# Optimization experiments

Hardware: AMD Instinct MI355X
Metric: run time of the kernel (lower is better)

The kernel has to match this reference:

```python
import jax, jax.numpy as jnp
import numpy as np

ALPHA_LO = float(np.exp(-1.0 / 5.0))   # 0.81873...
ALPHA_HI = float(np.exp(-1.0 / 25.0))  # 0.96079...
T_CROP = 0


def setup_inputs() -> dict:
    key = jax.random.key(0)
    k1, k2, k3, k4 = jax.random.split(key, 4)
    B, T, I, H = 64, 2000, 512, 512
    x = jax.random.normal(k1, (B, T, I), dtype=jnp.float32)
    # W ~ U(-sqrt(1/I), sqrt(1/I)) per nn.init.uniform_
    lim = float(np.sqrt(1.0 / I))
    W = jax.random.uniform(k2, (H, I), dtype=jnp.float32, minval=-lim, maxval=lim)
    # alpha ~ U(alpha_lim[0], alpha_lim[1])
    alpha = jax.random.uniform(k3, (H,), dtype=jnp.float32, minval=ALPHA_LO, maxval=ALPHA_HI)
    # initial membrane potential ~ U(0,1) (torch.rand in _readout_cell)
    u0 = jax.random.uniform(k4, (B, H), dtype=jnp.float32)
    return {"x": x, "W": W, "alpha": alpha, "u0": u0}


def reference(x, W, alpha, u0):
    # x: [B, T, I], W: [H, I] -> Wx: [B, T, H]
    alpha_c = jnp.clip(alpha, ALPHA_LO, ALPHA_HI)  # [H]
    beta = 1.0 - alpha_c                           # [H]
    Wx = jnp.einsum("bti,hi->bth", x, W)          # [B, T, H]
    Wx_t = jnp.swapaxes(Wx, 0, 1)                  # [T, B, H] for scan

    out0 = jnp.zeros_like(u0)

    def step(carry, inp):
        ut, out, t = carry
        wx_t = inp  # [B, H]
        ut = alpha_c * ut + beta * wx_t
        out = out + jnp.where(t >= T_CROP, jax.nn.softmax(ut, axis=1), 0.0)
        return (ut, out, t + 1), None

    (_, out, _), _ = jax.lax.scan(step, (u0, out0, jnp.int32(0)), Wx_t)
    return out  # [B, H]
```

## Files before the change

kernel.cpp:

```cpp
#include <hip/hip_runtime.h>
#include <hip/hip_bf16.h>
#include <stdint.h>

#define ALPHA_LO 0.8187307530779818f
#define ALPHA_HI 0.9607894391523232f

#define BATCH 64
#define TT    2000
#define II    512
#define HH    512
#define MM    (BATCH*TT)
#define LCH   50
#define CCH   (TT/LCH)

typedef __bf16 bf16;
typedef bf16  bf16x8 __attribute__((ext_vector_type(8)));
typedef float f32x4  __attribute__((ext_vector_type(4)));

#define GLDS(src, dst) __builtin_amdgcn_global_load_lds( \
    (const __attribute__((address_space(1))) unsigned int*)(src), \
    (__attribute__((address_space(3))) unsigned int*)(dst), 16, 0, 0)

__global__ void k_convW(const float* __restrict__ W, bf16* __restrict__ Wbt) {
    const int t  = blockIdx.x * 256 + threadIdx.x;
    const int h  = t >> 6;
    const int kb = t & 63;
    const float* src = W + (size_t)h * II + kb * 8;
    float4 v0 = *(const float4*)(src);
    float4 v1 = *(const float4*)(src + 4);
    bf16x8 o;
    o[0]=(bf16)v0.x; o[1]=(bf16)v0.y; o[2]=(bf16)v0.z; o[3]=(bf16)v0.w;
    o[4]=(bf16)v1.x; o[5]=(bf16)v1.y; o[6]=(bf16)v1.z; o[7]=(bf16)v1.w;
    const int ks = kb >> 2, kq = kb & 3, jj = h >> 4, fr = h & 15;
    bf16* dst = Wbt + (size_t)ks * 16384 + jj * 512 + kq * 128 + fr * 8;
    *(bf16x8*)dst = o;
}

__global__ __launch_bounds__(512, 2) void k_gemm(const float* __restrict__ X,
                                                 const bf16* __restrict__ Wbt,
                                                 bf16* __restrict__ Y) {
    __shared__ bf16 Al[2][4096];
    __shared__ bf16 Bl[4][16384];
    const int tid  = threadIdx.x;
    const int m0   = blockIdx.x * 128;
    const int lane = tid & 63;
    const int wv   = tid >> 6;
    const int wr   = (wv >> 2) * 64;
    const int wcj  = (wv & 3) * 8;
    const int wblk = (wv >> 2) * 4;
    const int fr   = lane & 15;
    const int kq   = lane >> 4;

    f32x4 acc[4][8] = {};

    const int arow = ((tid >> 6) << 4) + (tid & 15);
    const int akq  = (tid >> 4) & 3;
    const float* xa = X + (size_t)(m0 + arow) * II + akq * 8;
    const int aoff = tid * 8;

    const bf16* wsrc = Wbt + wv * 512 + lane * 8;

    float4 av[3][2];

    #pragma unroll
    for (int q = 0; q < 4; ++q) GLDS(wsrc + q * 4096,         &Bl[0][(q * 8 + wv) * 512]);
    av[0][0] = *(const float4*)(xa);
    av[0][1] = *(const float4*)(xa + 4);
    #pragma unroll
    for (int q = 0; q < 4; ++q) GLDS(wsrc + 16384 + q * 4096, &Bl[1][(q * 8 + wv) * 512]);
    av[1][0] = *(const float4*)(xa + 32);
    av[1][1] = *(const float4*)(xa + 36);

    #pragma unroll
    for (int ks = 0; ks < 16; ++ks) {
        const int bcur = ks & 3;
        const int acur = ks & 1;
        const int rcur = ks % 3;
        if (ks + 2 < 16) {
            #pragma unroll
            for (int q = 0; q < 4; ++q)
                GLDS(wsrc + (size_t)(ks + 2) * 16384 + q * 4096,
                     &Bl[(ks + 2) & 3][(q * 8 + wv) * 512]);
            av[(ks + 2) % 3][0] = *(const float4*)(xa + (size_t)(ks + 2) * 32);
            av[(ks + 2) % 3][1] = *(const float4*)(xa + (size_t)(ks + 2) * 32 + 4);
        }
        float4 a0 = av[rcur][0], a1 = av[rcur][1];
        bf16x8 c;
        c[0]=(bf16)a0.x; c[1]=(bf16)a0.y; c[2]=(bf16)a0.z; c[3]=(bf16)a0.w;
        c[4]=(bf16)a1.x; c[5]=(bf16)a1.y; c[6]=(bf16)a1.z; c[7]=(bf16)a1.w;
        *(bf16x8*)(&Al[acur][aoff]) = c;
        asm volatile("s_waitcnt lgkmcnt(0)" ::: "memory");
        __builtin_amdgcn_s_barrier();
        bf16x8 af[4], bb[8];
        #pragma unroll
        for (int i = 0; i < 4; ++i)
            af[i] = *(const bf16x8*)(&Al[acur][(wblk + i) * 512 + lane * 8]);
        #pragma unroll
        for (int j = 0; j < 8; ++j)
            bb[j] = *(const bf16x8*)(&Bl[bcur][(wcj + j) * 512 + lane * 8]);
        __builtin_amdgcn_s_setprio(1);
        #pragma unroll
        for (int i = 0; i < 4; ++i)
            #pragma unroll
            for (int j = 0; j < 8; ++j)
                acc[i][j] = __builtin_amdgcn_mfma_f32_16x16x32_bf16(af[i], bb[j], acc[i][j], 0, 0, 0);
        __builtin_amdgcn_s_setprio(0);
        asm volatile("" ::: "memory");
    }

    #pragma unroll
    for (int i = 0; i < 4; ++i)
        #pragma unroll
        for (int j = 0; j < 8; ++j) {
            const int row = m0 + wr + i * 16 + kq * 4;
            const int col = (wcj + j) * 16 + fr;
            #pragma unroll
            for (int r = 0; r < 4; ++r)
                Y[(size_t)(row + r) * HH + col] = (bf16)acc[i][j][r];
        }
}

__global__ void k_chunk(const bf16* __restrict__ Y, const float* __restrict__ alpha,
                        float* __restrict__ P) {
    const int c = blockIdx.x, b = blockIdx.y;
    const int lane = threadIdx.x;
    const int h0 = lane * 8;
    float a[8], p[8];
    #pragma unroll
    for (int k = 0; k < 8; ++k) {
        a[k] = fminf(fmaxf(alpha[h0 + k], ALPHA_LO), ALPHA_HI);
        p[k] = 0.f;
    }
    const bf16* base = Y + ((size_t)b * TT + (size_t)c * LCH) * HH + h0;
    for (int j = 0; j < LCH; ++j) {
        bf16x8 w = *(const bf16x8*)(base + (size_t)j * HH);
        #pragma unroll
        for (int k = 0; k < 8; ++k) p[k] = a[k] * p[k] + (float)w[k];
    }
    float* po = P + ((size_t)c * BATCH + b) * HH + h0;
    #pragma unroll
    for (int k = 0; k < 8; ++k) po[k] = (1.f - a[k]) * p[k];
}

__global__ void k_prefix(const float* __restrict__ alpha, const float* __restrict__ u0,
                         const float* __restrict__ P, float* __restrict__ V) {
    const int g = blockIdx.x * 256 + threadIdx.x;
    const int h = g & (HH - 1);
    float a = fminf(fmaxf(alpha[h], ALPHA_LO), ALPHA_HI);
    float a2 = a * a, a4 = a2 * a2, a5 = a4 * a;
    float b2 = a5 * a5, b4 = b2 * b2, a25 = b4 * a5;
    float aL = a25 * a25;
    float v = u0[g];
    for (int c = 0; c < CCH; ++c) {
        const size_t idx = (size_t)c * (BATCH * HH) + g;
        V[idx] = v;
        v = aL * v + P[idx];
    }
}

__global__ void k_soft(const bf16* __restrict__ Y, const float* __restrict__ alpha,
                       const float* __restrict__ V, float* __restrict__ OutP) {
    const int c = blockIdx.x, b = blockIdx.y;
    const int lane = threadIdx.x;
    const int h0 = lane * 8;
    float a[8], bt[8], u[8], o[8];
    #pragma unroll
    for (int k = 0; k < 8; ++k) {
        a[k]  = fminf(fmaxf(alpha[h0 + k], ALPHA_LO), ALPHA_HI);
        bt[k] = 1.f - a[k];
        o[k]  = 0.f;
    }
    const float* vb = V + ((size_t)c * BATCH + b) * HH + h0;
    #pragma unroll
    for (int k = 0; k < 8; ++k) u[k] = vb[k];
    const bf16* base = Y + ((size_t)b * TT + (size_t)c * LCH) * HH + h0;
    for (int j = 0; j < LCH; ++j) {
        bf16x8 w = *(const bf16x8*)(base + (size_t)j * HH);
        float e[8], s = 0.f;
        #pragma unroll
        for (int k = 0; k < 8; ++k) {
            u[k] = a[k] * u[k] + bt[k] * (float)w[k];
            e[k] = __expf(u[k]);
            s += e[k];
        }
        #pragma unroll
        for (int off = 32; off >= 1; off >>= 1) s += __shfl_xor(s, off, 64);
        const float inv = 1.f / s;
        #pragma unroll
        for (int k = 0; k < 8; ++k) o[k] += e[k] * inv;
    }
    float* po = OutP + ((size_t)c * BATCH + b) * HH + h0;
    #pragma unroll
    for (int k = 0; k < 8; ++k) po[k] = o[k];
}

__global__ void k_reduce(const float* __restrict__ OutP, float* __restrict__ out) {
    const int g = blockIdx.x * 256 + threadIdx.x;
    float s = 0.f;
    for (int c = 0; c < CCH; ++c) s += OutP[(size_t)c * (BATCH * HH) + g];
    out[g] = s;
}

extern "C" void kernel_launch(void* const* d_in, const int* in_sizes, int n_in,
                              void* d_out, int out_size, void* d_ws, size_t ws_size,
                              hipStream_t stream) {
    const float* x     = (const float*)d_in[0];
    const float* W     = (const float*)d_in[1];
    const float* alpha = (const float*)d_in[2];
    const float* u0    = (const float*)d_in[3];
    float* out = (float*)d_out;

    char* ws = (char*)d_ws;
    bf16* Wbt = (bf16*)ws;
    bf16* Yx  = (bf16*)(ws + 524288);
    float* P  = (float*)(ws + 524288 + 131072000);
    float* V  = P + (size_t)CCH * BATCH * HH;
    float* OutP = V + (size_t)CCH * BATCH * HH;

    hipLaunchKernelGGL(k_convW,  dim3(128),          dim3(256), 0, stream, W, Wbt);
    hipLaunchKernelGGL(k_gemm,   dim3(MM / 128),     dim3(512), 0, stream, x, Wbt, Yx);
    hipLaunchKernelGGL(k_chunk,  dim3(CCH, BATCH),   dim3(64),  0, stream, Yx, alpha, P);
    hipLaunchKernelGGL(k_prefix, dim3(BATCH*HH/256), dim3(256), 0, stream, alpha, u0, P, V);
    hipLaunchKernelGGL(k_soft,   dim3(CCH, BATCH),   dim3(64),  0, stream, Yx, alpha, V, OutP);
    hipLaunchKernelGGL(k_reduce, dim3(BATCH*HH/256), dim3(256), 0, stream, OutP, out);
}
```

Baseline: 179.5 us.

## Split GEMM N dimension across blocks with XCD-aware swizzle and smaller LDS

```diff
diff --git a/kernel.cpp b/kernel.cpp
--- a/kernel.cpp
+++ b/kernel.cpp
@@ -36,68 +36,80 @@
     *(bf16x8*)dst = o;
 }
 
-__global__ __launch_bounds__(512, 2) void k_gemm(const float* __restrict__ X,
+__global__ __launch_bounds__(256, 2) void k_gemm(const float* __restrict__ X,
                                                  const bf16* __restrict__ Wbt,
                                                  bf16* __restrict__ Y) {
     __shared__ bf16 Al[2][4096];
-    __shared__ bf16 Bl[4][16384];
+    __shared__ bf16 Bl[3][8192];
     const int tid  = threadIdx.x;
-    const int m0   = blockIdx.x * 128;
+    const int swz  = (blockIdx.x & 7) * 250 + (blockIdx.x >> 3);
+    const int m0   = (swz >> 1) * 128;
+    const int nt   = swz & 1;
     const int lane = tid & 63;
     const int wv   = tid >> 6;
-    const int wr   = (wv >> 2) * 64;
-    const int wcj  = (wv & 3) * 8;
-    const int wblk = (wv >> 2) * 4;
-    const int fr   = lane & 15;
-    const int kq   = lane >> 4;
+    const int wm   = wv >> 1;
+    const int wn   = wv & 1;
 
     f32x4 acc[4][8] = {};
 
-    const int arow = ((tid >> 6) << 4) + (tid & 15);
+    const int fr0  = tid & 15;
     const int akq  = (tid >> 4) & 3;
-    const float* xa = X + (size_t)(m0 + arow) * II + akq * 8;
+    const int row0 = ((tid >> 6) << 4) + fr0;
+    const float* xa = X + (size_t)(m0 + row0) * II + akq * 8;
     const int aoff = tid * 8;
 
-    const bf16* wsrc = Wbt + wv * 512 + lane * 8;
-
-    float4 av[3][2];
-
-    #pragma unroll
-    for (int q = 0; q < 4; ++q) GLDS(wsrc + q * 4096,         &Bl[0][(q * 8 + wv) * 512]);
+    const bf16* bsrc = Wbt + nt * 8192 + lane * 8;
+
+    float4 av[3][4];
+
+    #pragma unroll
+    for (int q = 0; q < 4; ++q) GLDS(bsrc + (q * 4 + wv) * 512,         &Bl[0][(q * 4 + wv) * 512]);
     av[0][0] = *(const float4*)(xa);
     av[0][1] = *(const float4*)(xa + 4);
-    #pragma unroll
-    for (int q = 0; q < 4; ++q) GLDS(wsrc + 16384 + q * 4096, &Bl[1][(q * 8 + wv) * 512]);
+    av[0][2] = *(const float4*)(xa + 32768);
+    av[0][3] = *(const float4*)(xa + 32772);
+    #pragma unroll
+    for (int q = 0; q < 4; ++q) GLDS(bsrc + 16384 + (q * 4 + wv) * 512, &Bl[1][(q * 4 + wv) * 512]);
     av[1][0] = *(const float4*)(xa + 32);
     av[1][1] = *(const float4*)(xa + 36);
+    av[1][2] = *(const float4*)(xa + 32800);
+    av[1][3] = *(const float4*)(xa + 32804);
 
     #pragma unroll
     for (int ks = 0; ks < 16; ++ks) {
-        const int bcur = ks & 3;
+        const int bcur = ks % 3;
         const int acur = ks & 1;
-        const int rcur = ks % 3;
         if (ks + 2 < 16) {
+            const int nb = (ks + 2) % 3;
             #pragma unroll
             for (int q = 0; q < 4; ++q)
-                GLDS(wsrc + (size_t)(ks + 2) * 16384 + q * 4096,
-                     &Bl[(ks + 2) & 3][(q * 8 + wv) * 512]);
-            av[(ks + 2) % 3][0] = *(const float4*)(xa + (size_t)(ks + 2) * 32);
-            av[(ks + 2) % 3][1] = *(const float4*)(xa + (size_t)(ks + 2) * 32 + 4);
-        }
-        float4 a0 = av[rcur][0], a1 = av[rcur][1];
-        bf16x8 c;
-        c[0]=(bf16)a0.x; c[1]=(bf16)a0.y; c[2]=(bf16)a0.z; c[3]=(bf16)a0.w;
-        c[4]=(bf16)a1.x; c[5]=(bf16)a1.y; c[6]=(bf16)a1.z; c[7]=(bf16)a1.w;
-        *(bf16x8*)(&Al[acur][aoff]) = c;
+                GLDS(bsrc + (size_t)(ks + 2) * 16384 + (q * 4 + wv) * 512,
+                     &Bl[nb][(q * 4 + wv) * 512]);
+            av[nb][0] = *(const float4*)(xa + (size_t)(ks + 2) * 32);
+            av[nb][1] = *(const float4*)(xa + (size_t)(ks + 2) * 32 + 4);
+            av[nb][2] = *(const float4*)(xa + (size_t)(ks + 2) * 32 + 32768);
+            av[nb][3] = *(const float4*)(xa + (size_t)(ks + 2) * 32 + 32772);
+        }
+        {
+            float4 a0 = av[bcur][0], a1 = av[bcur][1];
+            float4 a2 = av[bcur][2], a3 = av[bcur][3];
+            bf16x8 c0, c1;
+            c0[0]=(bf16)a0.x; c0[1]=(bf16)a0.y; c0[2]=(bf16)a0.z; c0[3]=(bf16)a0.w;
+            c0[4]=(bf16)a1.x; c0[5]=(bf16)a1.y; c0[6]=(bf16)a1.z; c0[7]=(bf16)a1.w;
+            c1[0]=(bf16)a2.x; c1[1]=(bf16)a2.y; c1[2]=(bf16)a2.z; c1[3]=(bf16)a2.w;
+            c1[4]=(bf16)a3.x; c1[5]=(bf16)a3.y; c1[6]=(bf16)a3.z; c1[7]=(bf16)a3.w;
+            *(bf16x8*)(&Al[acur][aoff])        = c0;
+            *(bf16x8*)(&Al[acur][aoff + 2048]) = c1;
+        }
         asm volatile("s_waitcnt lgkmcnt(0)" ::: "memory");
         __builtin_amdgcn_s_barrier();
         bf16x8 af[4], bb[8];
         #pragma unroll
         for (int i = 0; i < 4; ++i)
-            af[i] = *(const bf16x8*)(&Al[acur][(wblk + i) * 512 + lane * 8]);
+            af[i] = *(const bf16x8*)(&Al[acur][(wm * 4 + i) * 512 + lane * 8]);
         #pragma unroll
         for (int j = 0; j < 8; ++j)
-            bb[j] = *(const bf16x8*)(&Bl[bcur][(wcj + j) * 512 + lane * 8]);
+            bb[j] = *(const bf16x8*)(&Bl[bcur][(wn * 8 + j) * 512 + lane * 8]);
         __builtin_amdgcn_s_setprio(1);
         #pragma unroll
         for (int i = 0; i < 4; ++i)
@@ -108,12 +120,14 @@
         asm volatile("" ::: "memory");
     }
 
+    const int fr = lane & 15;
+    const int kq = lane >> 4;
     #pragma unroll
     for (int i = 0; i < 4; ++i)
         #pragma unroll
         for (int j = 0; j < 8; ++j) {
-            const int row = m0 + wr + i * 16 + kq * 4;
-            const int col = (wcj + j) * 16 + fr;
+            const int row = m0 + wm * 64 + i * 16 + kq * 4;
+            const int col = nt * 256 + (wn * 8 + j) * 16 + fr;
             #pragma unroll
             for (int r = 0; r < 4; ++r)
                 Y[(size_t)(row + r) * HH + col] = (bf16)acc[i][j][r];
@@ -218,7 +232,7 @@
     float* OutP = V + (size_t)CCH * BATCH * HH;
 
     hipLaunchKernelGGL(k_convW,  dim3(128),          dim3(256), 0, stream, W, Wbt);
-    hipLaunchKernelGGL(k_gemm,   dim3(MM / 128),     dim3(512), 0, stream, x, Wbt, Yx);
+    hipLaunchKernelGGL(k_gemm,   dim3(2000),         dim3(256), 0, stream, x, Wbt, Yx);
     hipLaunchKernelGGL(k_chunk,  dim3(CCH, BATCH),   dim3(64),  0, stream, Yx, alpha, P);
     hipLaunchKernelGGL(k_prefix, dim3(BATCH*HH/256), dim3(256), 0, stream, alpha, u0, P, V);
     hipLaunchKernelGGL(k_soft,   dim3(CCH, BATCH),   dim3(64),  0, stream, Yx, alpha, V, OutP);
```

Result: slower. 213.3 us (+18.8%).
